# Optimization experiments

Measured on AMD Instinct MI355X. Metric: run time of the kernel, lower is better.

Reference implementation:

```python
import jax, jax.numpy as jnp
import numpy as np
from math import sqrt

B, N, D = 8, 4096, 512

def rotary(x, phases):
    # x: [B,N,D], phases: [B,N,D/2]
    c, s = jnp.cos(phases), jnp.sin(phases)
    a, b = jnp.split(x, 2, axis=-1)
    return jnp.concatenate([a * c - b * s, a * s + b * c], axis=-1)

def setup_inputs() -> dict:
    key = jax.random.key(0)
    ks = jax.random.split(key, 8)
    phi = jax.random.normal(ks[0], (B, N, D), dtype=jnp.float32)
    coords = jax.random.normal(ks[1], (B, N, 3), dtype=jnp.float32)
    weights = jax.random.uniform(ks[2], (B, N), dtype=jnp.float32)
    std = 1.0 / sqrt(D)
    Wq = jax.random.normal(ks[3], (D, D), dtype=jnp.float32) * std
    Wk = jax.random.normal(ks[4], (D, D), dtype=jnp.float32) * std
    Wv = jax.random.normal(ks[5], (D, D), dtype=jnp.float32) * std
    bq = jnp.zeros((D,), jnp.float32)
    bk = jnp.zeros((D,), jnp.float32)
    bv = jnp.zeros((D,), jnp.float32)
    # mode_lift weight, std = 1/kernel_scale with kernel_scale=1.0
    Wrot = jax.random.normal(ks[6], (D // 2, 3), dtype=jnp.float32)
    return {"phi": phi, "coords": coords, "weights": weights,
            "Wq": Wq, "bq": bq, "Wk": Wk, "bk": bk, "Wv": Wv, "bv": bv,
            "Wrot": Wrot}

def reference(phi, coords, weights, Wq, bq, Wk, bk, Wv, bv, Wrot):
    d = phi.shape[-1]
    q = phi @ Wq.T + bq
    k = phi @ Wk.T + bk
    v = phi @ Wv.T + bv
    # _normalize: scale query by 1/sqrt(d); attach quadrature weights to value
    q = q * (1.0 / sqrt(d))
    v = weights[..., None] * v
    # rotary positional encoding on q and k
    phases = jnp.einsum('bnc,dc->bnd', coords, Wrot)  # [B,N,D/2]
    q = rotary(q, phases)
    k = rotary(k, phases)
    # linear attention: q @ (k^T @ v), O(N*d^2)
    kv = jnp.einsum('bnd,bne->bde', k, v)   # [B,D,D]
    return jnp.einsum('bnd,bde->bne', q, kv)  # [B,N,D]
```

## Files before the change

### kernel.cpp

```cpp
#include <hip/hip_runtime.h>


typedef _Float16 f16x8 __attribute__((ext_vector_type(8)));
typedef _Float16 f16x4 __attribute__((ext_vector_type(4)));
typedef float f32x4 __attribute__((ext_vector_type(4)));

__device__ __forceinline__ void gl_lds16(const void* g, void* l) {
    __builtin_amdgcn_global_load_lds(
        (const __attribute__((address_space(1))) void*)g,
        (__attribute__((address_space(3))) void*)l, 16, 0, 0);
}

__device__ __forceinline__ void stage2(const _Float16* gA, size_t sA,
                                       const _Float16* gB, size_t sB,
                                       _Float16* As, _Float16* Bs,
                                       int ca, int srow, int sseg) {
    gl_lds16(&gA[(size_t)(ca * 16 + srow) * sA + sseg], &As[ca * 512]);
    gl_lds16(&gA[(size_t)(ca * 16 + 16 + srow) * sA + sseg], &As[(ca + 1) * 512]);
    gl_lds16(&gB[(size_t)(ca * 16 + srow) * sB + sseg], &Bs[ca * 512]);
    gl_lds16(&gB[(size_t)(ca * 16 + 16 + srow) * sB + sseg], &Bs[(ca + 1) * 512]);
}

__device__ __forceinline__ void mfma_step(const _Float16* As, const _Float16* Bs,
                                          int wm, int wn, int l16, int qs,
                                          f32x4 acc[4][4]) {
    f16x8 af[4], bf[4];
    #pragma unroll
    for (int mi = 0; mi < 4; mi++)
        af[mi] = *(const f16x8*)&As[(wm + mi * 16 + l16) * 32 + qs * 8];
    #pragma unroll
    for (int ni = 0; ni < 4; ni++)
        bf[ni] = *(const f16x8*)&Bs[(wn + ni * 16 + l16) * 32 + qs * 8];
    #pragma unroll
    for (int mi = 0; mi < 4; mi++)
        #pragma unroll
        for (int ni = 0; ni < 4; ni++)
            acc[mi][ni] = __builtin_amdgcn_mfma_f32_16x16x32_f16(
                af[mi], bf[ni], acc[mi][ni], 0, 0, 0);
}

#define PHASE(BUFA, BUFB, VM)                                                 \
    asm volatile("s_waitcnt vmcnt(" #VM ")" ::: "memory");                    \
    __builtin_amdgcn_s_barrier();                                             \
    asm volatile("" ::: "memory");                                            \
    __builtin_amdgcn_sched_barrier(0);                                        \
    mfma_step(BUFA, BUFB, wm, wn, l16, qs, acc);                              \
    asm volatile("s_waitcnt lgkmcnt(0)" ::: "memory");                        \
    __builtin_amdgcn_sched_barrier(0);                                        \
    __builtin_amdgcn_s_barrier();                                             \
    asm volatile("" ::: "memory");

#define PIPE_LOOP(gA, sA, gB, sB)                                             \
    stage2(gA, sA, gB, sB, As0, Bs0, ca, srow, sseg);                         \
    stage2(gA + 32, sA, gB + 32, sB, As1, Bs1, ca, srow, sseg);               \
    _Pragma("unroll")                                                         \
    for (int p = 0; p < 8; p++) {                                             \
        const int t0 = 2 * p;                                                 \
        PHASE(As0, Bs0, 4)                                                    \
        if (t0 + 2 < 16)                                                      \
            stage2(gA + (size_t)(t0 + 2) * 32, sA,                            \
                   gB + (size_t)(t0 + 2) * 32, sB,                            \
                   As0, Bs0, ca, srow, sseg);                                 \
        if (p < 7) { PHASE(As1, Bs1, 4) }                                     \
        else       { PHASE(As1, Bs1, 0) }                                     \
        if (t0 + 3 < 16)                                                      \
            stage2(gA + (size_t)(t0 + 3) * 32, sA,                            \
                   gB + (size_t)(t0 + 3) * 32, sB,                            \
                   As1, Bs1, ca, srow, sseg);                                 \
    }

__global__ __launch_bounds__(256) void convert_phi(const float* __restrict__ phi,
                                                   _Float16* __restrict__ phi_h) {
    int i = (blockIdx.x * 256 + threadIdx.x) * 4;
    float4 v = *(const float4*)(phi + i);
    f16x4 o = {(_Float16)v.x, (_Float16)v.y, (_Float16)v.z, (_Float16)v.w};
    *(f16x4*)(phi_h + i) = o;
}

__global__ __launch_bounds__(256) void pack_w(
    const float* __restrict__ Wq, const float* __restrict__ Wk,
    const float* __restrict__ Wv, const float* __restrict__ bq,
    const float* __restrict__ bk, const float* __restrict__ bv,
    _Float16* __restrict__ wcat, float* __restrict__ bcat) {
    int j = blockIdx.x;
    int reg = j >> 9, jr = j & 511;
    const float* W; const float* bias;
    if (reg == 0)      { W = Wq; bias = bq; }
    else if (reg == 1) { W = Wk; bias = bk; }
    else               { W = Wv; bias = bv; }
    int d = (reg < 2) ? ((jr & 1) ? (jr >> 1) + 256 : (jr >> 1)) : jr;
    for (int i = threadIdx.x; i < 512; i += 256)
        wcat[j * 512 + i] = (_Float16)W[d * 512 + i];
    if (threadIdx.x == 0) bcat[j] = bias[d];
}

__global__ __launch_bounds__(256) void qkv_kernel(
    const _Float16* __restrict__ phi_h, const _Float16* __restrict__ wcat,
    const float* __restrict__ bcat, const float* __restrict__ coords,
    const float* __restrict__ weights, const float* __restrict__ Wrot,
    _Float16* __restrict__ qr, _Float16* __restrict__ krT,
    _Float16* __restrict__ vwT) {
    __shared__ __align__(16) char smem[34816];
    _Float16* As0 = (_Float16*)smem;
    _Float16* Bs0 = (_Float16*)(smem + 8192);
    _Float16* As1 = (_Float16*)(smem + 16384);
    _Float16* Bs1 = (_Float16*)(smem + 24576);
    _Float16* Ts  = (_Float16*)smem;

    const int tid = threadIdx.x;
    const int lane = tid & 63, wave = tid >> 6;
    const int quad = lane >> 4, l16 = lane & 15;
    const int qs = quad ^ ((l16 >> 1) & 3);
    const int wm = (wave >> 1) * 64, wn = (wave & 1) * 64;
    const int m0 = blockIdx.y * 128;
    const int c0 = blockIdx.x * 128;
    const int ca = wave * 2;
    const int srow = lane >> 2;
    const int sseg = (((lane & 3) ^ ((lane >> 3) & 3)) * 8);

    const _Float16* gA = phi_h + (size_t)m0 * 512;
    const _Float16* gB = wcat + (size_t)c0 * 512;

    f32x4 acc[4][4] = {};

    PIPE_LOOP(gA, 512, gB, 512)

    const int region = c0 >> 9;
    const float qscale = 0.04419417382415922f;

    float bias[4], w0[4], w1[4], w2[4];
    #pragma unroll
    for (int ni = 0; ni < 4; ni++) {
        int gc = c0 + wn + ni * 16 + l16;
        bias[ni] = bcat[gc];
        if (region < 2) {
            int jp = (gc & 511) >> 1;
            w0[ni] = Wrot[jp * 3];
            w1[ni] = Wrot[jp * 3 + 1];
            w2[ni] = Wrot[jp * 3 + 2];
        }
    }

    if (region == 0) {
        #pragma unroll
        for (int mi = 0; mi < 4; mi++)
            #pragma unroll
            for (int r = 0; r < 4; r++) {
                int row = wm + mi * 16 + quad * 4 + r;
                int gm = m0 + row;
                float x = coords[gm * 3], y = coords[gm * 3 + 1], z = coords[gm * 3 + 2];
                #pragma unroll
                for (int ni = 0; ni < 4; ni++) {
                    float val = (acc[mi][ni][r] + bias[ni]) * qscale;
                    float part = __shfl_xor(val, 1);
                    float ph = x * w0[ni] + y * w1[ni] + z * w2[ni];
                    float sv, cv; __sincosf(ph, &sv, &cv);
                    float res = (l16 & 1) ? (part * sv + val * cv)
                                          : (val * cv - part * sv);
                    Ts[row * 136 + wn + ni * 16 + l16] = (_Float16)res;
                }
            }
        __syncthreads();
        for (int i = tid; i < 2048; i += 256) {
            int row = i >> 4, cv = (i & 15) * 8;
            *(f16x8*)&qr[(m0 + row) * 512 + c0 + cv] = *(f16x8*)&Ts[row * 136 + cv];
        }
    } else {
        #pragma unroll
        for (int mi = 0; mi < 4; mi++)
            #pragma unroll
            for (int r = 0; r < 4; r++) {
                int row = wm + mi * 16 + quad * 4 + r;
                int gm = m0 + row;
                if (region == 1) {
                    float x = coords[gm * 3], y = coords[gm * 3 + 1], z = coords[gm * 3 + 2];
                    #pragma unroll
                    for (int ni = 0; ni < 4; ni++) {
                        float val = acc[mi][ni][r] + bias[ni];
                        float part = __shfl_xor(val, 1);
                        float ph = x * w0[ni] + y * w1[ni] + z * w2[ni];
                        float sv, cv; __sincosf(ph, &sv, &cv);
                        float res = (l16 & 1) ? (part * sv + val * cv)
                                              : (val * cv - part * sv);
                        Ts[(wn + ni * 16 + l16) * 136 + row] = (_Float16)res;
                    }
                } else {
                    float wgt = weights[gm];
                    #pragma unroll
                    for (int ni = 0; ni < 4; ni++) {
                        float val = (acc[mi][ni][r] + bias[ni]) * wgt;
                        Ts[(wn + ni * 16 + l16) * 136 + row] = (_Float16)val;
                    }
                }
            }
        __syncthreads();
        _Float16* dst = (region == 1) ? krT : vwT;
        const int b = m0 >> 12, n0 = m0 & 4095, cb = c0 & 511;
        for (int i = tid; i < 2048; i += 256) {
            int col = i >> 4, rv = (i & 15) * 8;
            *(f16x8*)&dst[((size_t)b * 512 + cb + col) * 4096 + n0 + rv] =
                *(f16x8*)&Ts[col * 136 + rv];
        }
    }
}

__global__ __launch_bounds__(256) void kv_kernel(
    const _Float16* __restrict__ vwT, const _Float16* __restrict__ krT,
    _Float16* __restrict__ kvp) {
    __shared__ __align__(16) char smem[32768];
    _Float16* As0 = (_Float16*)smem;
    _Float16* Bs0 = (_Float16*)(smem + 8192);
    _Float16* As1 = (_Float16*)(smem + 16384);
    _Float16* Bs1 = (_Float16*)(smem + 24576);
    const int tid = threadIdx.x, lane = tid & 63, wave = tid >> 6;
    const int quad = lane >> 4, l16 = lane & 15;
    const int qs = quad ^ ((l16 >> 1) & 3);
    const int wm = (wave >> 1) * 64, wn = (wave & 1) * 64;
    const int d0 = blockIdx.x * 128, e0 = blockIdx.y * 128;
    const int b = blockIdx.z >> 3, split = blockIdx.z & 7;
    const int ca = wave * 2;
    const int srow = lane >> 2;
    const int sseg = (((lane & 3) ^ ((lane >> 3) & 3)) * 8);
    const size_t base = (size_t)b * 512 * 4096;
    const int kbeg = split * 512;
    const _Float16* gA = vwT + base + (size_t)e0 * 4096 + kbeg;
    const _Float16* gB = krT + base + (size_t)d0 * 4096 + kbeg;
    f32x4 acc[4][4] = {};

    PIPE_LOOP(gA, 4096, gB, 4096)

    _Float16* dst = kvp + ((size_t)split * 8 + b) * 262144;
    #pragma unroll
    for (int mi = 0; mi < 4; mi++)
        #pragma unroll
        for (int ni = 0; ni < 4; ni++)
            #pragma unroll
            for (int r = 0; r < 4; r++) {
                int e = e0 + wm + mi * 16 + quad * 4 + r;
                int d = d0 + wn + ni * 16 + l16;
                dst[e * 512 + d] = (_Float16)acc[mi][ni][r];
            }
}

__global__ __launch_bounds__(256) void reduce_kv(const _Float16* __restrict__ kvp,
                                                 _Float16* __restrict__ kvT) {
    int i = (blockIdx.x * 256 + threadIdx.x) * 8;
    float s[8] = {};
    #pragma unroll
    for (int sp = 0; sp < 8; sp++) {
        f16x8 v = *(const f16x8*)(kvp + (size_t)sp * 2097152 + i);
        #pragma unroll
        for (int j = 0; j < 8; j++) s[j] += (float)v[j];
    }
    f16x8 o;
    #pragma unroll
    for (int j = 0; j < 8; j++) o[j] = (_Float16)s[j];
    *(f16x8*)(kvT + i) = o;
}

__global__ __launch_bounds__(256) void out_kernel(
    const _Float16* __restrict__ qr, const _Float16* __restrict__ kvT,
    float* __restrict__ out) {
    __shared__ __align__(16) char smem[32768];
    _Float16* As0 = (_Float16*)smem;
    _Float16* Bs0 = (_Float16*)(smem + 8192);
    _Float16* As1 = (_Float16*)(smem + 16384);
    _Float16* Bs1 = (_Float16*)(smem + 24576);
    const int tid = threadIdx.x, lane = tid & 63, wave = tid >> 6;
    const int quad = lane >> 4, l16 = lane & 15;
    const int qs = quad ^ ((l16 >> 1) & 3);
    const int wm = (wave >> 1) * 64, wn = (wave & 1) * 64;
    const int m0 = blockIdx.y * 128, e0 = blockIdx.x * 128;
    const int b = m0 >> 12;
    const int ca = wave * 2;
    const int srow = lane >> 2;
    const int sseg = (((lane & 3) ^ ((lane >> 3) & 3)) * 8);
    const _Float16* gA = qr + (size_t)m0 * 512;
    const _Float16* gB = kvT + (size_t)b * 262144 + (size_t)e0 * 512;
    f32x4 acc[4][4] = {};

    PIPE_LOOP(gA, 512, gB, 512)

    #pragma unroll
    for (int mi = 0; mi < 4; mi++)
        #pragma unroll
        for (int ni = 0; ni < 4; ni++)
            #pragma unroll
            for (int r = 0; r < 4; r++) {
                int gm = m0 + wm + mi * 16 + quad * 4 + r;
                int e = e0 + wn + ni * 16 + l16;
                out[(size_t)gm * 512 + e] = acc[mi][ni][r];
            }
}

extern "C" void kernel_launch(void* const* d_in, const int* in_sizes, int n_in,
                              void* d_out, int out_size, void* d_ws, size_t ws_size,
                              hipStream_t stream) {
    const float* phi     = (const float*)d_in[0];
    const float* coords  = (const float*)d_in[1];
    const float* weights = (const float*)d_in[2];
    const float* Wq      = (const float*)d_in[3];
    const float* bq      = (const float*)d_in[4];
    const float* Wk      = (const float*)d_in[5];
    const float* bk      = (const float*)d_in[6];
    const float* Wv      = (const float*)d_in[7];
    const float* bv      = (const float*)d_in[8];
    const float* Wrot    = (const float*)d_in[9];
    float* out = (float*)d_out;

    char* ws = (char*)d_ws;
    _Float16* phi_h = (_Float16*)(ws);
    _Float16* kvp   = (_Float16*)(ws);
    _Float16* wcat  = (_Float16*)(ws + 33554432);
    float*    bcat  = (float*)   (ws + 35127296);
    _Float16* qr    = (_Float16*)(ws + 35133440);
    _Float16* krT   = (_Float16*)(ws + 68687872);
    _Float16* vwT   = (_Float16*)(ws + 102242304);
    _Float16* kvT   = (_Float16*)(ws + 135796736);

    convert_phi<<<16384, 256, 0, stream>>>(phi, phi_h);
    pack_w<<<1536, 256, 0, stream>>>(Wq, Wk, Wv, bq, bk, bv, wcat, bcat);
    qkv_kernel<<<dim3(12, 256), 256, 0, stream>>>(phi_h, wcat, bcat, coords,
                                                  weights, Wrot, qr, krT, vwT);
    kv_kernel<<<dim3(4, 4, 64), 256, 0, stream>>>(vwT, krT, kvp);
    reduce_kv<<<1024, 256, 0, stream>>>(kvp, kvT);
    out_kernel<<<dim3(4, 256), 256, 0, stream>>>(qr, kvT, out);
}
```

Before: 310.9 us.

## Enlarge GEMM tiles to 256x256 with 512-thread blocks and 8x4 wave accumulators

Doubles the block tile in all three GEMM kernels from 128x128 to 256x256 using 8 waves, each holding a 128x64 accumulator. The qkv epilogue is restructured to process the two row halves in turn through a shared transpose buffer. The intent is better operand reuse and less global and LDS traffic per FLOP. In exchange, register pressure doubles and LDS use rises to 64-68 KB per block, which can reduce occupancy. Grid sizes also drop (e.g. kv_kernel to 256 blocks), which may underfill the GPU.

Measured after the change: 346.9 us. 11.5% more time.

```diff
diff --git a/kernel.cpp b/kernel.cpp
--- a/kernel.cpp
+++ b/kernel.cpp
@@ -23,16 +23,16 @@
 
 __device__ __forceinline__ void mfma_step(const _Float16* As, const _Float16* Bs,
                                           int wm, int wn, int l16, int qs,
-                                          f32x4 acc[4][4]) {
-    f16x8 af[4], bf[4];
-    #pragma unroll
-    for (int mi = 0; mi < 4; mi++)
+                                          f32x4 acc[8][4]) {
+    f16x8 af[8], bf[4];
+    #pragma unroll
+    for (int mi = 0; mi < 8; mi++)
         af[mi] = *(const f16x8*)&As[(wm + mi * 16 + l16) * 32 + qs * 8];
     #pragma unroll
     for (int ni = 0; ni < 4; ni++)
         bf[ni] = *(const f16x8*)&Bs[(wn + ni * 16 + l16) * 32 + qs * 8];
     #pragma unroll
-    for (int mi = 0; mi < 4; mi++)
+    for (int mi = 0; mi < 8; mi++)
         #pragma unroll
         for (int ni = 0; ni < 4; ni++)
             acc[mi][ni] = __builtin_amdgcn_mfma_f32_16x16x32_f16(
@@ -94,26 +94,27 @@
     if (threadIdx.x == 0) bcat[j] = bias[d];
 }
 
-__global__ __launch_bounds__(256) void qkv_kernel(
+__global__ __launch_bounds__(512) void qkv_kernel(
     const _Float16* __restrict__ phi_h, const _Float16* __restrict__ wcat,
     const float* __restrict__ bcat, const float* __restrict__ coords,
     const float* __restrict__ weights, const float* __restrict__ Wrot,
     _Float16* __restrict__ qr, _Float16* __restrict__ krT,
     _Float16* __restrict__ vwT) {
-    __shared__ __align__(16) char smem[34816];
+    __shared__ __align__(16) char smem[69632];
     _Float16* As0 = (_Float16*)smem;
-    _Float16* Bs0 = (_Float16*)(smem + 8192);
-    _Float16* As1 = (_Float16*)(smem + 16384);
-    _Float16* Bs1 = (_Float16*)(smem + 24576);
+    _Float16* Bs0 = (_Float16*)(smem + 16384);
+    _Float16* As1 = (_Float16*)(smem + 32768);
+    _Float16* Bs1 = (_Float16*)(smem + 49152);
     _Float16* Ts  = (_Float16*)smem;
 
     const int tid = threadIdx.x;
     const int lane = tid & 63, wave = tid >> 6;
     const int quad = lane >> 4, l16 = lane & 15;
     const int qs = quad ^ ((l16 >> 1) & 3);
-    const int wm = (wave >> 1) * 64, wn = (wave & 1) * 64;
-    const int m0 = blockIdx.y * 128;
-    const int c0 = blockIdx.x * 128;
+    const int wr = wave >> 2, wc = wave & 3;
+    const int wm = wr * 128, wn = wc * 64;
+    const int m0 = blockIdx.y * 256;
+    const int c0 = blockIdx.x * 256;
     const int ca = wave * 2;
     const int srow = lane >> 2;
     const int sseg = (((lane & 3) ^ ((lane >> 3) & 3)) * 8);
@@ -121,7 +122,7 @@
     const _Float16* gA = phi_h + (size_t)m0 * 512;
     const _Float16* gB = wcat + (size_t)c0 * 512;
 
-    f32x4 acc[4][4] = {};
+    f32x4 acc[8][4] = {};
 
     PIPE_LOOP(gA, 512, gB, 512)
 
@@ -141,82 +142,83 @@
         }
     }
 
-    if (region == 0) {
-        #pragma unroll
-        for (int mi = 0; mi < 4; mi++)
+    const int b = m0 >> 12, n0 = m0 & 4095, cb = c0 & 511;
+    _Float16* dstT = (region == 1) ? krT : vwT;
+    for (int rh = 0; rh < 2; rh++) {
+        if (rh) __syncthreads();
+        if (wr == rh) {
             #pragma unroll
-            for (int r = 0; r < 4; r++) {
-                int row = wm + mi * 16 + quad * 4 + r;
-                int gm = m0 + row;
-                float x = coords[gm * 3], y = coords[gm * 3 + 1], z = coords[gm * 3 + 2];
+            for (int mi = 0; mi < 8; mi++)
                 #pragma unroll
-                for (int ni = 0; ni < 4; ni++) {
-                    float val = (acc[mi][ni][r] + bias[ni]) * qscale;
-                    float part = __shfl_xor(val, 1);
-                    float ph = x * w0[ni] + y * w1[ni] + z * w2[ni];
-                    float sv, cv; __sincosf(ph, &sv, &cv);
-                    float res = (l16 & 1) ? (part * sv + val * cv)
-                                          : (val * cv - part * sv);
-                    Ts[row * 136 + wn + ni * 16 + l16] = (_Float16)res;
-                }
-            }
-        __syncthreads();
-        for (int i = tid; i < 2048; i += 256) {
-            int row = i >> 4, cv = (i & 15) * 8;
-            *(f16x8*)&qr[(m0 + row) * 512 + c0 + cv] = *(f16x8*)&Ts[row * 136 + cv];
-        }
-    } else {
-        #pragma unroll
-        for (int mi = 0; mi < 4; mi++)
-            #pragma unroll
-            for (int r = 0; r < 4; r++) {
-                int row = wm + mi * 16 + quad * 4 + r;
-                int gm = m0 + row;
-                if (region == 1) {
-                    float x = coords[gm * 3], y = coords[gm * 3 + 1], z = coords[gm * 3 + 2];
-                    #pragma unroll
-                    for (int ni = 0; ni < 4; ni++) {
-                        float val = acc[mi][ni][r] + bias[ni];
-                        float part = __shfl_xor(val, 1);
-                        float ph = x * w0[ni] + y * w1[ni] + z * w2[ni];
-                        float sv, cv; __sincosf(ph, &sv, &cv);
-                        float res = (l16 & 1) ? (part * sv + val * cv)
-                                              : (val * cv - part * sv);
-                        Ts[(wn + ni * 16 + l16) * 136 + row] = (_Float16)res;
-                    }
-                } else {
-                    float wgt = weights[gm];
-                    #pragma unroll
-                    for (int ni = 0; ni < 4; ni++) {
-                        float val = (acc[mi][ni][r] + bias[ni]) * wgt;
-                        Ts[(wn + ni * 16 + l16) * 136 + row] = (_Float16)val;
+                for (int r = 0; r < 4; r++) {
+                    int row = mi * 16 + quad * 4 + r;
+                    int gm = m0 + rh * 128 + row;
+                    if (region == 0) {
+                        float x = coords[gm * 3], y = coords[gm * 3 + 1],
+                              z = coords[gm * 3 + 2];
+                        #pragma unroll
+                        for (int ni = 0; ni < 4; ni++) {
+                            float val = (acc[mi][ni][r] + bias[ni]) * qscale;
+                            float part = __shfl_xor(val, 1);
+                            float ph = x * w0[ni] + y * w1[ni] + z * w2[ni];
+                            float sv, cv; __sincosf(ph, &sv, &cv);
+                            float res = (l16 & 1) ? (part * sv + val * cv)
+                                                  : (val * cv - part * sv);
+                            Ts[row * 264 + wn + ni * 16 + l16] = (_Float16)res;
+                        }
+                    } else if (region == 1) {
+                        float x = coords[gm * 3], y = coords[gm * 3 + 1],
+                              z = coords[gm * 3 + 2];
+                        #pragma unroll
+                        for (int ni = 0; ni < 4; ni++) {
+                            float val = acc[mi][ni][r] + bias[ni];
+                            float part = __shfl_xor(val, 1);
+                            float ph = x * w0[ni] + y * w1[ni] + z * w2[ni];
+                            float sv, cv; __sincosf(ph, &sv, &cv);
+                            float res = (l16 & 1) ? (part * sv + val * cv)
+                                                  : (val * cv - part * sv);
+                            Ts[(wn + ni * 16 + l16) * 136 + row] = (_Float16)res;
+                        }
+                    } else {
+                        float wgt = weights[gm];
+                        #pragma unroll
+                        for (int ni = 0; ni < 4; ni++) {
+                            float val = (acc[mi][ni][r] + bias[ni]) * wgt;
+                            Ts[(wn + ni * 16 + l16) * 136 + row] = (_Float16)val;
+                        }
                     }
                 }
+        }
+        __syncthreads();
+        if (region == 0) {
+            for (int i = tid; i < 4096; i += 512) {
+                int row = i >> 5, cv = (i & 31) * 8;
+                *(f16x8*)&qr[(size_t)(m0 + rh * 128 + row) * 512 + c0 + cv] =
+                    *(f16x8*)&Ts[row * 264 + cv];
             }
-        __syncthreads();
-        _Float16* dst = (region == 1) ? krT : vwT;
-        const int b = m0 >> 12, n0 = m0 & 4095, cb = c0 & 511;
-        for (int i = tid; i < 2048; i += 256) {
-            int col = i >> 4, rv = (i & 15) * 8;
-            *(f16x8*)&dst[((size_t)b * 512 + cb + col) * 4096 + n0 + rv] =
-                *(f16x8*)&Ts[col * 136 + rv];
+        } else {
+            for (int i = tid; i < 4096; i += 512) {
+                int col = i >> 4, rv = (i & 15) * 8;
+                *(f16x8*)&dstT[((size_t)b * 512 + cb + col) * 4096 +
+                               n0 + rh * 128 + rv] = *(f16x8*)&Ts[col * 136 + rv];
+            }
         }
     }
 }
 
-__global__ __launch_bounds__(256) void kv_kernel(
+__global__ __launch_bounds__(512) void kv_kernel(
     const _Float16* __restrict__ vwT, const _Float16* __restrict__ krT,
     _Float16* __restrict__ kvp) {
-    __shared__ __align__(16) char smem[32768];
+    __shared__ __align__(16) char smem[65536];
     _Float16* As0 = (_Float16*)smem;
-    _Float16* Bs0 = (_Float16*)(smem + 8192);
-    _Float16* As1 = (_Float16*)(smem + 16384);
-    _Float16* Bs1 = (_Float16*)(smem + 24576);
+    _Float16* Bs0 = (_Float16*)(smem + 16384);
+    _Float16* As1 = (_Float16*)(smem + 32768);
+    _Float16* Bs1 = (_Float16*)(smem + 49152);
     const int tid = threadIdx.x, lane = tid & 63, wave = tid >> 6;
     const int quad = lane >> 4, l16 = lane & 15;
     const int qs = quad ^ ((l16 >> 1) & 3);
-    const int wm = (wave >> 1) * 64, wn = (wave & 1) * 64;
-    const int d0 = blockIdx.x * 128, e0 = blockIdx.y * 128;
+    const int wm = (wave >> 2) * 128, wn = (wave & 3) * 64;
+    const int d0 = blockIdx.x * 256, e0 = blockIdx.y * 256;
     const int b = blockIdx.z >> 3, split = blockIdx.z & 7;
     const int ca = wave * 2;
     const int srow = lane >> 2;
@@ -225,13 +227,13 @@
     const int kbeg = split * 512;
     const _Float16* gA = vwT + base + (size_t)e0 * 4096 + kbeg;
     const _Float16* gB = krT + base + (size_t)d0 * 4096 + kbeg;
-    f32x4 acc[4][4] = {};
+    f32x4 acc[8][4] = {};
 
     PIPE_LOOP(gA, 4096, gB, 4096)
 
     _Float16* dst = kvp + ((size_t)split * 8 + b) * 262144;
     #pragma unroll
-    for (int mi = 0; mi < 4; mi++)
+    for (int mi = 0; mi < 8; mi++)
         #pragma unroll
         for (int ni = 0; ni < 4; ni++)
             #pragma unroll
@@ -258,31 +260,31 @@
     *(f16x8*)(kvT + i) = o;
 }
 
-__global__ __launch_bounds__(256) void out_kernel(
+__global__ __launch_bounds__(512) void out_kernel(
     const _Float16* __restrict__ qr, const _Float16* __restrict__ kvT,
     float* __restrict__ out) {
-    __shared__ __align__(16) char smem[32768];
+    __shared__ __align__(16) char smem[65536];
     _Float16* As0 = (_Float16*)smem;
-    _Float16* Bs0 = (_Float16*)(smem + 8192);
-    _Float16* As1 = (_Float16*)(smem + 16384);
-    _Float16* Bs1 = (_Float16*)(smem + 24576);
+    _Float16* Bs0 = (_Float16*)(smem + 16384);
+    _Float16* As1 = (_Float16*)(smem + 32768);
+    _Float16* Bs1 = (_Float16*)(smem + 49152);
     const int tid = threadIdx.x, lane = tid & 63, wave = tid >> 6;
     const int quad = lane >> 4, l16 = lane & 15;
     const int qs = quad ^ ((l16 >> 1) & 3);
-    const int wm = (wave >> 1) * 64, wn = (wave & 1) * 64;
-    const int m0 = blockIdx.y * 128, e0 = blockIdx.x * 128;
+    const int wm = (wave >> 2) * 128, wn = (wave & 3) * 64;
+    const int m0 = blockIdx.y * 256, e0 = blockIdx.x * 256;
     const int b = m0 >> 12;
     const int ca = wave * 2;
     const int srow = lane >> 2;
     const int sseg = (((lane & 3) ^ ((lane >> 3) & 3)) * 8);
     const _Float16* gA = qr + (size_t)m0 * 512;
     const _Float16* gB = kvT + (size_t)b * 262144 + (size_t)e0 * 512;
-    f32x4 acc[4][4] = {};
+    f32x4 acc[8][4] = {};
 
     PIPE_LOOP(gA, 512, gB, 512)
 
     #pragma unroll
-    for (int mi = 0; mi < 4; mi++)
+    for (int mi = 0; mi < 8; mi++)
         #pragma unroll
         for (int ni = 0; ni < 4; ni++)
             #pragma unroll
@@ -320,9 +322,9 @@
 
     convert_phi<<<16384, 256, 0, stream>>>(phi, phi_h);
     pack_w<<<1536, 256, 0, stream>>>(Wq, Wk, Wv, bq, bk, bv, wcat, bcat);
-    qkv_kernel<<<dim3(12, 256), 256, 0, stream>>>(phi_h, wcat, bcat, coords,
-                                                  weights, Wrot, qr, krT, vwT);
-    kv_kernel<<<dim3(4, 4, 64), 256, 0, stream>>>(vwT, krT, kvp);
+    qkv_kernel<<<dim3(6, 128), 512, 0, stream>>>(phi_h, wcat, bcat, coords,
+                                                 weights, Wrot, qr, krT, vwT);
+    kv_kernel<<<dim3(2, 2, 64), 512, 0, stream>>>(vwT, krT, kvp);
     reduce_kv<<<1024, 256, 0, stream>>>(kvp, kvT);
-    out_kernel<<<dim3(4, 256), 256, 0, stream>>>(qr, kvT, out);
-}
+    out_kernel<<<dim3(2, 128), 512, 0, stream>>>(qr, kvT, out);
+}
```
